# Kernel optimization log

Hardware: AMD Instinct MI355X
Metric: run time of the kernel (lower is better)

## Reference

```python
import jax, jax.numpy as jnp
import numpy as np

HEADS = 8

def _ape(f, c):
    # sinusoidal positional encoding, matches PositionalEncoding buffer pe[:f]
    pos = jnp.arange(f, dtype=jnp.float32)[:, None]                      # [f,1]
    div = jnp.exp(jnp.arange(0, c, 2, dtype=jnp.float32) * (-np.log(10000.0) / c))  # [c/2]
    pe = jnp.zeros((f, c), dtype=jnp.float32)
    pe = pe.at[:, 0::2].set(jnp.sin(pos * div))
    pe = pe.at[:, 1::2].set(jnp.cos(pos * div))
    return pe


def setup_inputs() -> dict:
    key = jax.random.key(0)
    ks = jax.random.split(key, 6)
    b, f, d, c = 2, 16, 4096, 320
    s = 1.0 / np.sqrt(c)
    return {
        'hidden_states': jax.random.normal(ks[0], (b * f, d, c), dtype=jnp.float32),
        'Wq': jax.random.normal(ks[1], (c, c), dtype=jnp.float32) * s,
        'Wk': jax.random.normal(ks[2], (c, c), dtype=jnp.float32) * s,
        'Wv': jax.random.normal(ks[3], (c, c), dtype=jnp.float32) * s,
        'Wo': jax.random.normal(ks[4], (c, c), dtype=jnp.float32) * s,
        'bo': jnp.zeros((c,), dtype=jnp.float32),
        'video_length': 16,
    }


def reference(hidden_states, Wq, Wk, Wv, Wo, bo, video_length):
    bf, d, c = hidden_states.shape
    f = video_length
    b = bf // f
    dh = c // HEADS
    # rearrange '(b f) d c -> (b d) f c'
    x = hidden_states.reshape(b, f, d, c).transpose(0, 2, 1, 3).reshape(b * d, f, c)
    # APE positional encoding over frames (dropout p=0)
    x = x + _ape(f, c)[None, :, :]
    # QKV projections (bias-free, diffusers CrossAttention)
    q = (x @ Wq.T).reshape(b * d, f, HEADS, dh)
    k = (x @ Wk.T).reshape(b * d, f, HEADS, dh)
    v = (x @ Wv.T).reshape(b * d, f, HEADS, dh)
    scale = dh ** -0.5
    scores = jnp.einsum('bqhd,bkhd->bhqk', q, k) * scale          # [B,h,f,f]
    causal = jnp.tril(jnp.ones((f, f), dtype=bool))
    scores = jnp.where(causal[None, None], scores, -jnp.inf)
    attn = jax.nn.softmax(scores, axis=-1)
    out = jnp.einsum('bhqk,bkhd->bqhd', attn, v).reshape(b * d, f, c)
    out = out @ Wo.T + bo
    # rearrange '(b d) f c -> (b f) d c'
    out = out.reshape(b, d, f, c).transpose(0, 2, 1, 3).reshape(b * f, d, c)
    return out
```

## Files before the change

### kernel.cpp

```cpp
#include <hip/hip_runtime.h>
#include <stdint.h>

#define F 16
#define CDIM 320
#define DDIM 4096
#define NSEQ 8192
#define WPB 4
#define THREADS 256
#define NT 20
#define KS 10

typedef __attribute__((ext_vector_type(8))) short short8;
typedef __attribute__((ext_vector_type(4))) float f32x4;
typedef __attribute__((ext_vector_type(2))) unsigned int uint2v;
typedef __attribute__((ext_vector_type(4))) unsigned int uint4v;

__device__ __forceinline__ unsigned short f2bf(float f) {
    union { float f; uint32_t u; } v; v.f = f;
    uint32_t r = v.u + 0x7FFFu + ((v.u >> 16) & 1u);
    return (unsigned short)(r >> 16);
}
__device__ __forceinline__ int swz(int row, int b) {
    return row * 640 + (b ^ ((row & 7) << 4));
}

__global__ __launch_bounds__(256)
void pack_weights_kernel(const float* __restrict__ Wq, const float* __restrict__ Wk,
                         const float* __restrict__ Wv, const float* __restrict__ Wo,
                         char* __restrict__ pk)
{
    const int t = blockIdx.x * 256 + threadIdx.x;
    if (t >= 4 * NT * KS * 64) return;
    const int lane = t & 63;
    const int rest = t >> 6;
    const int ks = rest % KS;
    const int nt = (rest / KS) % NT;
    const int m  = rest / (KS * NT);
    const float* W = (m == 0) ? Wq : (m == 1) ? Wk : (m == 2) ? Wv : Wo;
    const int g = lane >> 4, lr = lane & 15;
    const float* src = W + (size_t)(nt * 16 + lr) * CDIM + ks * 32 + g * 8;
    const f32x4 a = *(const f32x4*)src;
    const f32x4 b = *(const f32x4*)(src + 4);
    float vals[8] = {a[0], a[1], a[2], a[3], b[0], b[1], b[2], b[3]};
    short8 o;
#pragma unroll
    for (int j = 0; j < 8; ++j) o[j] = (short)f2bf(vals[j]);
    *(short8*)(pk + (size_t)t * 16) = o;
}

__global__ __launch_bounds__(THREADS, 2)
void temporal_attn_kernel(const float* __restrict__ hs,
                          const char* __restrict__ wpk,
                          const float* __restrict__ bo,
                          float* __restrict__ out)
{
    extern __shared__ __align__(16) char smem[];
    const int tid  = threadIdx.x;
    const int lane = tid & 63;
    const int wave = tid >> 6;
    const int g    = lane >> 4;
    const int lr   = lane & 15;

    const int seq = blockIdx.x * WPB + wave;
    const int bi  = seq >> 12;
    const int di  = seq & (DDIM - 1);

    char* const kbuf = smem + wave * 20480;
    char* const vbuf = kbuf + 10240;
    const char* const wl = wpk + lane * 16;

    const float* xrow = hs + ((size_t)(bi * F + lr) * DDIM + di) * CDIM;
    short8 axk[KS];
#pragma unroll
    for (int ks = 0; ks < KS; ++ks) {
        const int k0 = ks * 32 + g * 8;
        const f32x4 a = __builtin_nontemporal_load((const f32x4*)(xrow + k0));
        const f32x4 b = __builtin_nontemporal_load((const f32x4*)(xrow + k0 + 4));
        float xv[8] = {a[0], a[1], a[2], a[3], b[0], b[1], b[2], b[3]};
#pragma unroll
        for (int jj = 0; jj < 4; ++jj) {
            const float c0 = (float)(k0 + 2 * jj);
            const float dv = __expf(c0 * -0.028782313662425575f);
            const float ang = (float)lr * dv;
            xv[2 * jj]     += __sinf(ang);
            xv[2 * jj + 1] += __cosf(ang);
        }
        short8 t;
#pragma unroll
        for (int j = 0; j < 8; ++j) t[j] = (short)f2bf(xv[j]);
        axk[ks] = t;
    }

    auto proj = [&](int m, char* dst, int mode) {
        const char* base = wpk + lane * 16 + (size_t)(m * NT) * KS * 1024;
        short8 fa[KS], fb[KS];
#pragma unroll
        for (int ks = 0; ks < KS; ++ks)
            fa[ks] = *(const short8*)(base + (size_t)ks * 1024);
#pragma unroll 1
        for (int np = 0; np < 10; ++np) {
#pragma unroll
            for (int ks = 0; ks < KS; ++ks)
                fb[ks] = *(const short8*)(base + (size_t)((2 * np + 1) * KS + ks) * 1024);
            f32x4 a0l = {0.f, 0.f, 0.f, 0.f}, a0h = {0.f, 0.f, 0.f, 0.f};
#pragma unroll
            for (int k5 = 0; k5 < 5; ++k5) {
                a0l = __builtin_amdgcn_mfma_f32_16x16x32_bf16(axk[k5],     fa[k5],     a0l, 0, 0, 0);
                a0h = __builtin_amdgcn_mfma_f32_16x16x32_bf16(axk[k5 + 5], fa[k5 + 5], a0h, 0, 0, 0);
            }
            const f32x4 a0 = a0l + a0h;
            if (np < 9) {
#pragma unroll
                for (int ks = 0; ks < KS; ++ks)
                    fa[ks] = *(const short8*)(base + (size_t)((2 * np + 2) * KS + ks) * 1024);
            }
            f32x4 a1l = {0.f, 0.f, 0.f, 0.f}, a1h = {0.f, 0.f, 0.f, 0.f};
#pragma unroll
            for (int k5 = 0; k5 < 5; ++k5) {
                a1l = __builtin_amdgcn_mfma_f32_16x16x32_bf16(axk[k5],     fb[k5],     a1l, 0, 0, 0);
                a1h = __builtin_amdgcn_mfma_f32_16x16x32_bf16(axk[k5 + 5], fb[k5 + 5], a1h, 0, 0, 0);
            }
            const f32x4 a1 = a1l + a1h;
            const int c0 = 2 * np * 16 + lr;
            const int c1 = c0 + 16;
            if (mode == 0) {
#pragma unroll
                for (int r = 0; r < 4; ++r) {
                    const int row = g * 4 + r;
                    *(short*)(dst + swz(row, c0 * 2)) = (short)f2bf(a0[r]);
                    *(short*)(dst + swz(row, c1 * 2)) = (short)f2bf(a1[r]);
                }
            } else {
#pragma unroll
                for (int r = 0; r < 4; ++r) {
                    const int key = g * 4 + r;
                    *(short*)(dst + c0 * 32 + key * 2) = (short)f2bf(a0[r]);
                    *(short*)(dst + c1 * 32 + key * 2) = (short)f2bf(a1[r]);
                }
            }
        }
    };

    proj(0, kbuf, 0);
    proj(1, vbuf, 0);

    const float scale = 0.15811388300841897f;
    const short8 z8 = {0, 0, 0, 0, 0, 0, 0, 0};
    uint2v ppk[8];
#pragma unroll
    for (int h = 0; h < 8; ++h) {
        const int cb = h * 80;
        short8 kf = *(const short8*)(vbuf + swz(lr, cb + g * 16));
        short8 qf = *(const short8*)(kbuf + swz(lr, cb + g * 16));
        short8 kt8 = *(const short8*)(vbuf + swz(lr, cb + 64));
        short8 qt8 = *(const short8*)(kbuf + swz(lr, cb + 64));
        short8 kt = (g == 0) ? kt8 : z8;
        short8 qt = (g == 0) ? qt8 : z8;
        f32x4 c = {0.f, 0.f, 0.f, 0.f};
        c = __builtin_amdgcn_mfma_f32_16x16x32_bf16(kf, qf, c, 0, 0, 0);
        c = __builtin_amdgcn_mfma_f32_16x16x32_bf16(kt, qt, c, 0, 0, 0);
        float sv[4];
        float m4 = -1e30f;
#pragma unroll
        for (int r = 0; r < 4; ++r) {
            sv[r] = (g * 4 + r <= lr) ? c[r] * scale : -1e30f;
            m4 = fmaxf(m4, sv[r]);
        }
        m4 = fmaxf(m4, __shfl_xor(m4, 16));
        m4 = fmaxf(m4, __shfl_xor(m4, 32));
        float sum = 0.f;
#pragma unroll
        for (int r = 0; r < 4; ++r) { sv[r] = __expf(sv[r] - m4); sum += sv[r]; }
        sum += __shfl_xor(sum, 16);
        sum += __shfl_xor(sum, 32);
        const float inv = 1.f / sum;
        uint2v pk;
        pk[0] = (uint32_t)f2bf(sv[0] * inv) | ((uint32_t)f2bf(sv[1] * inv) << 16);
        pk[1] = (uint32_t)f2bf(sv[2] * inv) | ((uint32_t)f2bf(sv[3] * inv) << 16);
        ppk[h] = pk;
    }

    proj(2, kbuf, 1);

#pragma unroll
    for (int h = 0; h < 8; ++h) {
        uint2v own = ppk[h];
        uint2v x16;
        x16[0] = (uint32_t)__shfl_xor((int)own[0], 16);
        x16[1] = (uint32_t)__shfl_xor((int)own[1], 16);
        uint4v pair;
        pair[0] = ((g & 1) == 0) ? own[0] : x16[0];
        pair[1] = ((g & 1) == 0) ? own[1] : x16[1];
        pair[2] = ((g & 1) == 0) ? x16[0] : own[0];
        pair[3] = ((g & 1) == 0) ? x16[1] : own[1];
        uint4v rec;
#pragma unroll
        for (int i = 0; i < 4; ++i) rec[i] = (uint32_t)__shfl_xor((int)pair[i], 32);
        uint4v af4;
#pragma unroll
        for (int i = 0; i < 4; ++i)
            af4[i] = (g == 0) ? pair[i] : (g == 1) ? rec[i] : 0u;
        const short8 af = *(const short8*)&af4;

#pragma unroll
        for (int t = 0; t < 3; ++t) {
            const int lcol = (t == 2) ? (lr & 7) : lr;
            const int col  = h * 40 + t * 16 + lcol;
            const short8 bf = *(const short8*)(kbuf + col * 32 + g * 16);
            f32x4 o = {0.f, 0.f, 0.f, 0.f};
            o = __builtin_amdgcn_mfma_f32_16x16x32_bf16(af, bf, o, 0, 0, 0);
            if (t < 2 || lr < 8) {
#pragma unroll
                for (int r = 0; r < 4; ++r)
                    *(short*)(vbuf + swz(g * 4 + r, col * 2)) = (short)f2bf(o[r]);
            }
        }
    }

    short8 aof[KS];
#pragma unroll
    for (int ks = 0; ks < KS; ++ks)
        aof[ks] = *(const short8*)(vbuf + swz(lr, ks * 64 + g * 16));

    {
        const char* base = wpk + lane * 16 + (size_t)(3 * NT) * KS * 1024;
        short8 fa[KS], fb[KS];
#pragma unroll
        for (int ks = 0; ks < KS; ++ks)
            fa[ks] = *(const short8*)(base + (size_t)ks * 1024);
#pragma unroll 1
        for (int np = 0; np < 10; ++np) {
#pragma unroll
            for (int ks = 0; ks < KS; ++ks)
                fb[ks] = *(const short8*)(base + (size_t)((2 * np + 1) * KS + ks) * 1024);
            f32x4 a0l = {0.f, 0.f, 0.f, 0.f}, a0h = {0.f, 0.f, 0.f, 0.f};
#pragma unroll
            for (int k5 = 0; k5 < 5; ++k5) {
                a0l = __builtin_amdgcn_mfma_f32_16x16x32_bf16(aof[k5],     fa[k5],     a0l, 0, 0, 0);
                a0h = __builtin_amdgcn_mfma_f32_16x16x32_bf16(aof[k5 + 5], fa[k5 + 5], a0h, 0, 0, 0);
            }
            const f32x4 a0 = a0l + a0h;
            if (np < 9) {
#pragma unroll
                for (int ks = 0; ks < KS; ++ks)
                    fa[ks] = *(const short8*)(base + (size_t)((2 * np + 2) * KS + ks) * 1024);
            }
            f32x4 a1l = {0.f, 0.f, 0.f, 0.f}, a1h = {0.f, 0.f, 0.f, 0.f};
#pragma unroll
            for (int k5 = 0; k5 < 5; ++k5) {
                a1l = __builtin_amdgcn_mfma_f32_16x16x32_bf16(aof[k5],     fb[k5],     a1l, 0, 0, 0);
                a1h = __builtin_amdgcn_mfma_f32_16x16x32_bf16(aof[k5 + 5], fb[k5 + 5], a1h, 0, 0, 0);
            }
            const f32x4 a1 = a1l + a1h;

            const int c0 = 2 * np * 16 + lr;
            const int c1 = c0 + 16;
            const float bias0 = bo[c0];
            const float bias1 = bo[c1];
#pragma unroll
            for (int r = 0; r < 4; ++r) {
                float* rowp = out + ((size_t)(bi * F + g * 4 + r) * DDIM + di) * CDIM;
                rowp[c0] = a0[r] + bias0;
                rowp[c1] = a1[r] + bias1;
            }
        }
    }
}

extern "C" void kernel_launch(void* const* d_in, const int* in_sizes, int n_in,
                              void* d_out, int out_size, void* d_ws, size_t ws_size,
                              hipStream_t stream) {
    const float* hs = (const float*)d_in[0];
    const float* Wq = (const float*)d_in[1];
    const float* Wk = (const float*)d_in[2];
    const float* Wv = (const float*)d_in[3];
    const float* Wo = (const float*)d_in[4];
    const float* bo = (const float*)d_in[5];
    float* out = (float*)d_out;
    char* wpk = (char*)d_ws;

    pack_weights_kernel<<<dim3((4 * NT * KS * 64 + 255) / 256), dim3(256), 0, stream>>>(
        Wq, Wk, Wv, Wo, wpk);

    const int lds = WPB * 20480;
    (void)hipFuncSetAttribute((const void*)temporal_attn_kernel,
                              hipFuncAttributeMaxDynamicSharedMemorySize, lds);
    temporal_attn_kernel<<<dim3(NSEQ / WPB), dim3(THREADS), lds, stream>>>(
        hs, wpk, bo, out);
}
```

Before: 252.5 us.

## Process two sequences per wave to reuse weight fragments across both

Each wave now handles two adjacent sequences (A and B) instead of one, so every weight fragment loaded from global memory feeds two MFMA chains and weight traffic per sequence is halved. The block shrinks to two waves with the same LDS per block, and launch bounds drop to one block minimum. The positional-encoding sin/cos is shared between the two sequences. The cost is much higher register pressure (two sets of activation fragments and accumulators), which may lower occupancy or cause spills. Each K-reduction also becomes a single serial MFMA chain of ten instead of two interleaved chains of five, though the A and B chains interleave with each other.

```diff
diff --git a/kernel.cpp b/kernel.cpp
--- a/kernel.cpp
+++ b/kernel.cpp
@@ -5,8 +5,7 @@
 #define CDIM 320
 #define DDIM 4096
 #define NSEQ 8192
-#define WPB 4
-#define THREADS 256
+#define THREADS 128
 #define NT 20
 #define KS 10
 
@@ -48,7 +47,7 @@
     *(short8*)(pk + (size_t)t * 16) = o;
 }
 
-__global__ __launch_bounds__(THREADS, 2)
+__global__ __launch_bounds__(THREADS, 1)
 void temporal_attn_kernel(const float* __restrict__ hs,
                           const char* __restrict__ wpk,
                           const float* __restrict__ bo,
@@ -61,37 +60,43 @@
     const int g    = lane >> 4;
     const int lr   = lane & 15;
 
-    const int seq = blockIdx.x * WPB + wave;
-    const int bi  = seq >> 12;
-    const int di  = seq & (DDIM - 1);
-
-    char* const kbuf = smem + wave * 20480;
-    char* const vbuf = kbuf + 10240;
-    const char* const wl = wpk + lane * 16;
-
-    const float* xrow = hs + ((size_t)(bi * F + lr) * DDIM + di) * CDIM;
-    short8 axk[KS];
+    const int seqA = blockIdx.x * 4 + wave * 2;
+    const int bi  = seqA >> 12;
+    const int di  = seqA & (DDIM - 1);
+
+    char* const kbufA = smem + wave * 40960;
+    char* const vbufA = kbufA + 10240;
+    char* const kbufB = kbufA + 20480;
+    char* const vbufB = kbufA + 30720;
+
+    const float* xrowA = hs + ((size_t)(bi * F + lr) * DDIM + di) * CDIM;
+    const float* xrowB = xrowA + CDIM;
+    short8 axkA[KS], axkB[KS];
 #pragma unroll
     for (int ks = 0; ks < KS; ++ks) {
         const int k0 = ks * 32 + g * 8;
-        const f32x4 a = __builtin_nontemporal_load((const f32x4*)(xrow + k0));
-        const f32x4 b = __builtin_nontemporal_load((const f32x4*)(xrow + k0 + 4));
-        float xv[8] = {a[0], a[1], a[2], a[3], b[0], b[1], b[2], b[3]};
+        const f32x4 aA = __builtin_nontemporal_load((const f32x4*)(xrowA + k0));
+        const f32x4 bA = __builtin_nontemporal_load((const f32x4*)(xrowA + k0 + 4));
+        const f32x4 aB = __builtin_nontemporal_load((const f32x4*)(xrowB + k0));
+        const f32x4 bB = __builtin_nontemporal_load((const f32x4*)(xrowB + k0 + 4));
+        float xvA[8] = {aA[0], aA[1], aA[2], aA[3], bA[0], bA[1], bA[2], bA[3]};
+        float xvB[8] = {aB[0], aB[1], aB[2], aB[3], bB[0], bB[1], bB[2], bB[3]};
 #pragma unroll
         for (int jj = 0; jj < 4; ++jj) {
             const float c0 = (float)(k0 + 2 * jj);
             const float dv = __expf(c0 * -0.028782313662425575f);
             const float ang = (float)lr * dv;
-            xv[2 * jj]     += __sinf(ang);
-            xv[2 * jj + 1] += __cosf(ang);
-        }
-        short8 t;
-#pragma unroll
-        for (int j = 0; j < 8; ++j) t[j] = (short)f2bf(xv[j]);
-        axk[ks] = t;
-    }
-
-    auto proj = [&](int m, char* dst, int mode) {
+            const float sn = __sinf(ang), cs = __cosf(ang);
+            xvA[2 * jj] += sn;  xvA[2 * jj + 1] += cs;
+            xvB[2 * jj] += sn;  xvB[2 * jj + 1] += cs;
+        }
+        short8 tA, tB;
+#pragma unroll
+        for (int j = 0; j < 8; ++j) { tA[j] = (short)f2bf(xvA[j]); tB[j] = (short)f2bf(xvB[j]); }
+        axkA[ks] = tA;  axkB[ks] = tB;
+    }
+
+    auto proj = [&](int m, char* dA, char* dB, int mode) {
         const char* base = wpk + lane * 16 + (size_t)(m * NT) * KS * 1024;
         short8 fa[KS], fb[KS];
 #pragma unroll
@@ -102,65 +107,66 @@
 #pragma unroll
             for (int ks = 0; ks < KS; ++ks)
                 fb[ks] = *(const short8*)(base + (size_t)((2 * np + 1) * KS + ks) * 1024);
-            f32x4 a0l = {0.f, 0.f, 0.f, 0.f}, a0h = {0.f, 0.f, 0.f, 0.f};
-#pragma unroll
-            for (int k5 = 0; k5 < 5; ++k5) {
-                a0l = __builtin_amdgcn_mfma_f32_16x16x32_bf16(axk[k5],     fa[k5],     a0l, 0, 0, 0);
-                a0h = __builtin_amdgcn_mfma_f32_16x16x32_bf16(axk[k5 + 5], fa[k5 + 5], a0h, 0, 0, 0);
-            }
-            const f32x4 a0 = a0l + a0h;
+            f32x4 a0A = {0.f, 0.f, 0.f, 0.f}, a0B = {0.f, 0.f, 0.f, 0.f};
+#pragma unroll
+            for (int ks = 0; ks < KS; ++ks) {
+                a0A = __builtin_amdgcn_mfma_f32_16x16x32_bf16(axkA[ks], fa[ks], a0A, 0, 0, 0);
+                a0B = __builtin_amdgcn_mfma_f32_16x16x32_bf16(axkB[ks], fa[ks], a0B, 0, 0, 0);
+            }
             if (np < 9) {
 #pragma unroll
                 for (int ks = 0; ks < KS; ++ks)
                     fa[ks] = *(const short8*)(base + (size_t)((2 * np + 2) * KS + ks) * 1024);
             }
-            f32x4 a1l = {0.f, 0.f, 0.f, 0.f}, a1h = {0.f, 0.f, 0.f, 0.f};
-#pragma unroll
-            for (int k5 = 0; k5 < 5; ++k5) {
-                a1l = __builtin_amdgcn_mfma_f32_16x16x32_bf16(axk[k5],     fb[k5],     a1l, 0, 0, 0);
-                a1h = __builtin_amdgcn_mfma_f32_16x16x32_bf16(axk[k5 + 5], fb[k5 + 5], a1h, 0, 0, 0);
-            }
-            const f32x4 a1 = a1l + a1h;
+            f32x4 a1A = {0.f, 0.f, 0.f, 0.f}, a1B = {0.f, 0.f, 0.f, 0.f};
+#pragma unroll
+            for (int ks = 0; ks < KS; ++ks) {
+                a1A = __builtin_amdgcn_mfma_f32_16x16x32_bf16(axkA[ks], fb[ks], a1A, 0, 0, 0);
+                a1B = __builtin_amdgcn_mfma_f32_16x16x32_bf16(axkB[ks], fb[ks], a1B, 0, 0, 0);
+            }
             const int c0 = 2 * np * 16 + lr;
             const int c1 = c0 + 16;
             if (mode == 0) {
 #pragma unroll
                 for (int r = 0; r < 4; ++r) {
                     const int row = g * 4 + r;
-                    *(short*)(dst + swz(row, c0 * 2)) = (short)f2bf(a0[r]);
-                    *(short*)(dst + swz(row, c1 * 2)) = (short)f2bf(a1[r]);
+                    *(short*)(dA + swz(row, c0 * 2)) = (short)f2bf(a0A[r]);
+                    *(short*)(dA + swz(row, c1 * 2)) = (short)f2bf(a1A[r]);
+                    *(short*)(dB + swz(row, c0 * 2)) = (short)f2bf(a0B[r]);
+                    *(short*)(dB + swz(row, c1 * 2)) = (short)f2bf(a1B[r]);
                 }
             } else {
 #pragma unroll
                 for (int r = 0; r < 4; ++r) {
                     const int key = g * 4 + r;
-                    *(short*)(dst + c0 * 32 + key * 2) = (short)f2bf(a0[r]);
-                    *(short*)(dst + c1 * 32 + key * 2) = (short)f2bf(a1[r]);
+                    *(short*)(dA + c0 * 32 + key * 2) = (short)f2bf(a0A[r]);
+                    *(short*)(dA + c1 * 32 + key * 2) = (short)f2bf(a1A[r]);
+                    *(short*)(dB + c0 * 32 + key * 2) = (short)f2bf(a0B[r]);
+                    *(short*)(dB + c1 * 32 + key * 2) = (short)f2bf(a1B[r]);
                 }
             }
         }
     };
 
-    proj(0, kbuf, 0);
-    proj(1, vbuf, 0);
+    proj(0, kbufA, kbufB, 0);
+    proj(1, vbufA, vbufB, 0);
 
     const float scale = 0.15811388300841897f;
     const short8 z8 = {0, 0, 0, 0, 0, 0, 0, 0};
-    uint2v ppk[8];
+    uint2v ppkA[8], ppkB[8];
 #pragma unroll
     for (int h = 0; h < 8; ++h) {
         const int cb = h * 80;
-        short8 kf = *(const short8*)(vbuf + swz(lr, cb + g * 16));
-        short8 qf = *(const short8*)(kbuf + swz(lr, cb + g * 16));
-        short8 kt8 = *(const short8*)(vbuf + swz(lr, cb + 64));
-        short8 qt8 = *(const short8*)(kbuf + swz(lr, cb + 64));
+        short8 kf = *(const short8*)(vbufA + swz(lr, cb + g * 16));
+        short8 qf = *(const short8*)(kbufA + swz(lr, cb + g * 16));
+        short8 kt8 = *(const short8*)(vbufA + swz(lr, cb + 64));
+        short8 qt8 = *(const short8*)(kbufA + swz(lr, cb + 64));
         short8 kt = (g == 0) ? kt8 : z8;
         short8 qt = (g == 0) ? qt8 : z8;
         f32x4 c = {0.f, 0.f, 0.f, 0.f};
         c = __builtin_amdgcn_mfma_f32_16x16x32_bf16(kf, qf, c, 0, 0, 0);
         c = __builtin_amdgcn_mfma_f32_16x16x32_bf16(kt, qt, c, 0, 0, 0);
-        float sv[4];
-        float m4 = -1e30f;
+        float sv[4]; float m4 = -1e30f;
 #pragma unroll
         for (int r = 0; r < 4; ++r) {
             sv[r] = (g * 4 + r <= lr) ? c[r] * scale : -1e30f;
@@ -177,14 +183,45 @@
         uint2v pk;
         pk[0] = (uint32_t)f2bf(sv[0] * inv) | ((uint32_t)f2bf(sv[1] * inv) << 16);
         pk[1] = (uint32_t)f2bf(sv[2] * inv) | ((uint32_t)f2bf(sv[3] * inv) << 16);
-        ppk[h] = pk;
-    }
-
-    proj(2, kbuf, 1);
-
+        ppkA[h] = pk;
+    }
 #pragma unroll
     for (int h = 0; h < 8; ++h) {
-        uint2v own = ppk[h];
+        const int cb = h * 80;
+        short8 kf = *(const short8*)(vbufB + swz(lr, cb + g * 16));
+        short8 qf = *(const short8*)(kbufB + swz(lr, cb + g * 16));
+        short8 kt8 = *(const short8*)(vbufB + swz(lr, cb + 64));
+        short8 qt8 = *(const short8*)(kbufB + swz(lr, cb + 64));
+        short8 kt = (g == 0) ? kt8 : z8;
+        short8 qt = (g == 0) ? qt8 : z8;
+        f32x4 c = {0.f, 0.f, 0.f, 0.f};
+        c = __builtin_amdgcn_mfma_f32_16x16x32_bf16(kf, qf, c, 0, 0, 0);
+        c = __builtin_amdgcn_mfma_f32_16x16x32_bf16(kt, qt, c, 0, 0, 0);
+        float sv[4]; float m4 = -1e30f;
+#pragma unroll
+        for (int r = 0; r < 4; ++r) {
+            sv[r] = (g * 4 + r <= lr) ? c[r] * scale : -1e30f;
+            m4 = fmaxf(m4, sv[r]);
+        }
+        m4 = fmaxf(m4, __shfl_xor(m4, 16));
+        m4 = fmaxf(m4, __shfl_xor(m4, 32));
+        float sum = 0.f;
+#pragma unroll
+        for (int r = 0; r < 4; ++r) { sv[r] = __expf(sv[r] - m4); sum += sv[r]; }
+        sum += __shfl_xor(sum, 16);
+        sum += __shfl_xor(sum, 32);
+        const float inv = 1.f / sum;
+        uint2v pk;
+        pk[0] = (uint32_t)f2bf(sv[0] * inv) | ((uint32_t)f2bf(sv[1] * inv) << 16);
+        pk[1] = (uint32_t)f2bf(sv[2] * inv) | ((uint32_t)f2bf(sv[3] * inv) << 16);
+        ppkB[h] = pk;
+    }
+
+    proj(2, kbufA, kbufB, 1);
+
+#pragma unroll
+    for (int h = 0; h < 8; ++h) {
+        uint2v own = ppkA[h];
         uint2v x16;
         x16[0] = (uint32_t)__shfl_xor((int)own[0], 16);
         x16[1] = (uint32_t)__shfl_xor((int)own[1], 16);
@@ -201,27 +238,60 @@
         for (int i = 0; i < 4; ++i)
             af4[i] = (g == 0) ? pair[i] : (g == 1) ? rec[i] : 0u;
         const short8 af = *(const short8*)&af4;
-
 #pragma unroll
         for (int t = 0; t < 3; ++t) {
             const int lcol = (t == 2) ? (lr & 7) : lr;
             const int col  = h * 40 + t * 16 + lcol;
-            const short8 bf = *(const short8*)(kbuf + col * 32 + g * 16);
+            const short8 bf = *(const short8*)(kbufA + col * 32 + g * 16);
             f32x4 o = {0.f, 0.f, 0.f, 0.f};
             o = __builtin_amdgcn_mfma_f32_16x16x32_bf16(af, bf, o, 0, 0, 0);
             if (t < 2 || lr < 8) {
 #pragma unroll
                 for (int r = 0; r < 4; ++r)
-                    *(short*)(vbuf + swz(g * 4 + r, col * 2)) = (short)f2bf(o[r]);
-            }
-        }
-    }
-
-    short8 aof[KS];
-#pragma unroll
-    for (int ks = 0; ks < KS; ++ks)
-        aof[ks] = *(const short8*)(vbuf + swz(lr, ks * 64 + g * 16));
-
+                    *(short*)(vbufA + swz(g * 4 + r, col * 2)) = (short)f2bf(o[r]);
+            }
+        }
+    }
+#pragma unroll
+    for (int h = 0; h < 8; ++h) {
+        uint2v own = ppkB[h];
+        uint2v x16;
+        x16[0] = (uint32_t)__shfl_xor((int)own[0], 16);
+        x16[1] = (uint32_t)__shfl_xor((int)own[1], 16);
+        uint4v pair;
+        pair[0] = ((g & 1) == 0) ? own[0] : x16[0];
+        pair[1] = ((g & 1) == 0) ? own[1] : x16[1];
+        pair[2] = ((g & 1) == 0) ? x16[0] : own[0];
+        pair[3] = ((g & 1) == 0) ? x16[1] : own[1];
+        uint4v rec;
+#pragma unroll
+        for (int i = 0; i < 4; ++i) rec[i] = (uint32_t)__shfl_xor((int)pair[i], 32);
+        uint4v af4;
+#pragma unroll
+        for (int i = 0; i < 4; ++i)
+            af4[i] = (g == 0) ? pair[i] : (g == 1) ? rec[i] : 0u;
+        const short8 af = *(const short8*)&af4;
+#pragma unroll
+        for (int t = 0; t < 3; ++t) {
+            const int lcol = (t == 2) ? (lr & 7) : lr;
+            const int col  = h * 40 + t * 16 + lcol;
+            const short8 bf = *(const short8*)(kbufB + col * 32 + g * 16);
+            f32x4 o = {0.f, 0.f, 0.f, 0.f};
+            o = __builtin_amdgcn_mfma_f32_16x16x32_bf16(af, bf, o, 0, 0, 0);
+            if (t < 2 || lr < 8) {
+#pragma unroll
+                for (int r = 0; r < 4; ++r)
+                    *(short*)(vbufB + swz(g * 4 + r, col * 2)) = (short)f2bf(o[r]);
+            }
+        }
+    }
+
+    short8 aofA[KS], aofB[KS];
+#pragma unroll
+    for (int ks = 0; ks < KS; ++ks) {
+        aofA[ks] = *(const short8*)(vbufA + swz(lr, ks * 64 + g * 16));
+        aofB[ks] = *(const short8*)(vbufB + swz(lr, ks * 64 + g * 16));
+    }
     {
         const char* base = wpk + lane * 16 + (size_t)(3 * NT) * KS * 1024;
         short8 fa[KS], fb[KS];
@@ -233,35 +303,35 @@
 #pragma unroll
             for (int ks = 0; ks < KS; ++ks)
                 fb[ks] = *(const short8*)(base + (size_t)((2 * np + 1) * KS + ks) * 1024);
-            f32x4 a0l = {0.f, 0.f, 0.f, 0.f}, a0h = {0.f, 0.f, 0.f, 0.f};
-#pragma unroll
-            for (int k5 = 0; k5 < 5; ++k5) {
-                a0l = __builtin_amdgcn_mfma_f32_16x16x32_bf16(aof[k5],     fa[k5],     a0l, 0, 0, 0);
-                a0h = __builtin_amdgcn_mfma_f32_16x16x32_bf16(aof[k5 + 5], fa[k5 + 5], a0h, 0, 0, 0);
-            }
-            const f32x4 a0 = a0l + a0h;
+            f32x4 a0A = {0.f, 0.f, 0.f, 0.f}, a0B = {0.f, 0.f, 0.f, 0.f};
+#pragma unroll
+            for (int ks = 0; ks < KS; ++ks) {
+                a0A = __builtin_amdgcn_mfma_f32_16x16x32_bf16(aofA[ks], fa[ks], a0A, 0, 0, 0);
+                a0B = __builtin_amdgcn_mfma_f32_16x16x32_bf16(aofB[ks], fa[ks], a0B, 0, 0, 0);
+            }
             if (np < 9) {
 #pragma unroll
                 for (int ks = 0; ks < KS; ++ks)
                     fa[ks] = *(const short8*)(base + (size_t)((2 * np + 2) * KS + ks) * 1024);
             }
-            f32x4 a1l = {0.f, 0.f, 0.f, 0.f}, a1h = {0.f, 0.f, 0.f, 0.f};
-#pragma unroll
-            for (int k5 = 0; k5 < 5; ++k5) {
-                a1l = __builtin_amdgcn_mfma_f32_16x16x32_bf16(aof[k5],     fb[k5],     a1l, 0, 0, 0);
-                a1h = __builtin_amdgcn_mfma_f32_16x16x32_bf16(aof[k5 + 5], fb[k5 + 5], a1h, 0, 0, 0);
-            }
-            const f32x4 a1 = a1l + a1h;
-
+            f32x4 a1A = {0.f, 0.f, 0.f, 0.f}, a1B = {0.f, 0.f, 0.f, 0.f};
+#pragma unroll
+            for (int ks = 0; ks < KS; ++ks) {
+                a1A = __builtin_amdgcn_mfma_f32_16x16x32_bf16(aofA[ks], fb[ks], a1A, 0, 0, 0);
+                a1B = __builtin_amdgcn_mfma_f32_16x16x32_bf16(aofB[ks], fb[ks], a1B, 0, 0, 0);
+            }
             const int c0 = 2 * np * 16 + lr;
             const int c1 = c0 + 16;
             const float bias0 = bo[c0];
             const float bias1 = bo[c1];
 #pragma unroll
             for (int r = 0; r < 4; ++r) {
-                float* rowp = out + ((size_t)(bi * F + g * 4 + r) * DDIM + di) * CDIM;
-                rowp[c0] = a0[r] + bias0;
-                rowp[c1] = a1[r] + bias1;
+                float* rowpA = out + ((size_t)(bi * F + g * 4 + r) * DDIM + di) * CDIM;
+                float* rowpB = rowpA + CDIM;
+                rowpA[c0] = a0A[r] + bias0;
+                rowpA[c1] = a1A[r] + bias1;
+                rowpB[c0] = a0B[r] + bias0;
+                rowpB[c1] = a1B[r] + bias1;
             }
         }
     }
@@ -282,9 +352,9 @@
     pack_weights_kernel<<<dim3((4 * NT * KS * 64 + 255) / 256), dim3(256), 0, stream>>>(
         Wq, Wk, Wv, Wo, wpk);
 
-    const int lds = WPB * 20480;
+    const int lds = 2 * 40960;
     (void)hipFuncSetAttribute((const void*)temporal_attn_kernel,
                               hipFuncAttributeMaxDynamicSharedMemorySize, lds);
-    temporal_attn_kernel<<<dim3(NSEQ / WPB), dim3(THREADS), lds, stream>>>(
+    temporal_attn_kernel<<<dim3(NSEQ / 4), dim3(THREADS), lds, stream>>>(
         hs, wpk, bo, out);
 }
```

After: 238.5 us. 1.06x faster.

## Process four sequences per wave to reuse weight fragments across sequences

Applied to the files above, without the earlier changes.

Each single-wave block now handles four sequences instead of one, so every weight fragment loaded from global memory feeds four MFMAs rather than one. The positional-encoding sin/cos values are computed once and shared across the four sequences. This cuts weight load traffic per sequence and gives more independent MFMA chains for latency hiding. The cost is much higher register pressure (four activation fragment sets plus four weight buffers), possible spills, and fewer waves per CU with 80KB LDS per single-wave block.

```diff
diff --git a/kernel.cpp b/kernel.cpp
--- a/kernel.cpp
+++ b/kernel.cpp
@@ -5,8 +5,8 @@
 #define CDIM 320
 #define DDIM 4096
 #define NSEQ 8192
-#define WPB 4
-#define THREADS 256
+#define SEQS 4
+#define THREADS 64
 #define NT 20
 #define KS 10
 
@@ -48,220 +48,279 @@
     *(short8*)(pk + (size_t)t * 16) = o;
 }
 
-__global__ __launch_bounds__(THREADS, 2)
+__global__ __launch_bounds__(THREADS, 1)
 void temporal_attn_kernel(const float* __restrict__ hs,
                           const char* __restrict__ wpk,
                           const float* __restrict__ bo,
                           float* __restrict__ out)
 {
     extern __shared__ __align__(16) char smem[];
-    const int tid  = threadIdx.x;
-    const int lane = tid & 63;
-    const int wave = tid >> 6;
+    const int lane = threadIdx.x & 63;
     const int g    = lane >> 4;
     const int lr   = lane & 15;
 
-    const int seq = blockIdx.x * WPB + wave;
-    const int bi  = seq >> 12;
-    const int di  = seq & (DDIM - 1);
-
-    char* const kbuf = smem + wave * 20480;
-    char* const vbuf = kbuf + 10240;
-    const char* const wl = wpk + lane * 16;
-
-    const float* xrow = hs + ((size_t)(bi * F + lr) * DDIM + di) * CDIM;
-    short8 axk[KS];
+    const int seq0 = blockIdx.x * SEQS;
+    const int bi  = seq0 >> 12;
+    const int di  = seq0 & (DDIM - 1);
+
+    char* kb[SEQS];
+    char* vb[SEQS];
+#pragma unroll
+    for (int s = 0; s < SEQS; ++s) {
+        kb[s] = smem + s * 20480;
+        vb[s] = kb[s] + 10240;
+    }
+
+    const float* xrow0 = hs + ((size_t)(bi * F + lr) * DDIM + di) * CDIM;
+    short8 axk[SEQS][KS];
 #pragma unroll
     for (int ks = 0; ks < KS; ++ks) {
         const int k0 = ks * 32 + g * 8;
-        const f32x4 a = __builtin_nontemporal_load((const f32x4*)(xrow + k0));
-        const f32x4 b = __builtin_nontemporal_load((const f32x4*)(xrow + k0 + 4));
-        float xv[8] = {a[0], a[1], a[2], a[3], b[0], b[1], b[2], b[3]};
+        float sn[4], cs[4];
 #pragma unroll
         for (int jj = 0; jj < 4; ++jj) {
             const float c0 = (float)(k0 + 2 * jj);
             const float dv = __expf(c0 * -0.028782313662425575f);
             const float ang = (float)lr * dv;
-            xv[2 * jj]     += __sinf(ang);
-            xv[2 * jj + 1] += __cosf(ang);
-        }
-        short8 t;
-#pragma unroll
-        for (int j = 0; j < 8; ++j) t[j] = (short)f2bf(xv[j]);
-        axk[ks] = t;
-    }
-
-    auto proj = [&](int m, char* dst, int mode) {
+            sn[jj] = __sinf(ang);  cs[jj] = __cosf(ang);
+        }
+#pragma unroll
+        for (int s = 0; s < SEQS; ++s) {
+            const float* xr = xrow0 + s * CDIM;
+            const f32x4 a = __builtin_nontemporal_load((const f32x4*)(xr + k0));
+            const f32x4 b = __builtin_nontemporal_load((const f32x4*)(xr + k0 + 4));
+            float xv[8] = {a[0], a[1], a[2], a[3], b[0], b[1], b[2], b[3]};
+#pragma unroll
+            for (int jj = 0; jj < 4; ++jj) {
+                xv[2 * jj]     += sn[jj];
+                xv[2 * jj + 1] += cs[jj];
+            }
+            short8 t;
+#pragma unroll
+            for (int j = 0; j < 8; ++j) t[j] = (short)f2bf(xv[j]);
+            axk[s][ks] = t;
+        }
+    }
+
+    auto proj = [&](int m, char* const* dst, int mode) {
         const char* base = wpk + lane * 16 + (size_t)(m * NT) * KS * 1024;
-        short8 fa[KS], fb[KS];
-#pragma unroll
-        for (int ks = 0; ks < KS; ++ks)
-            fa[ks] = *(const short8*)(base + (size_t)ks * 1024);
+        short8 f0[KS], f1[KS], f2[KS], f3[KS];
+#pragma unroll
+        for (int ks = 0; ks < KS; ++ks) {
+            f0[ks] = *(const short8*)(base + (size_t)ks * 1024);
+            f1[ks] = *(const short8*)(base + (size_t)(KS + ks) * 1024);
+        }
+        auto storeT = [&](int ti, const f32x4* acc) {
+            const int c = ti * 16 + lr;
+            if (mode == 0) {
+#pragma unroll
+                for (int s = 0; s < SEQS; ++s)
+#pragma unroll
+                    for (int r = 0; r < 4; ++r)
+                        *(short*)(dst[s] + swz(g * 4 + r, c * 2)) = (short)f2bf(acc[s][r]);
+            } else {
+#pragma unroll
+                for (int s = 0; s < SEQS; ++s)
+#pragma unroll
+                    for (int r = 0; r < 4; ++r)
+                        *(short*)(dst[s] + c * 32 + (g * 4 + r) * 2) = (short)f2bf(acc[s][r]);
+            }
+        };
 #pragma unroll 1
-        for (int np = 0; np < 10; ++np) {
-#pragma unroll
-            for (int ks = 0; ks < KS; ++ks)
-                fb[ks] = *(const short8*)(base + (size_t)((2 * np + 1) * KS + ks) * 1024);
-            f32x4 a0l = {0.f, 0.f, 0.f, 0.f}, a0h = {0.f, 0.f, 0.f, 0.f};
-#pragma unroll
-            for (int k5 = 0; k5 < 5; ++k5) {
-                a0l = __builtin_amdgcn_mfma_f32_16x16x32_bf16(axk[k5],     fa[k5],     a0l, 0, 0, 0);
-                a0h = __builtin_amdgcn_mfma_f32_16x16x32_bf16(axk[k5 + 5], fa[k5 + 5], a0h, 0, 0, 0);
-            }
-            const f32x4 a0 = a0l + a0h;
-            if (np < 9) {
+        for (int np2 = 0; np2 < 5; ++np2) {
+            const int t = np2 * 4;
+#pragma unroll
+            for (int ks = 0; ks < KS; ++ks) {
+                f2[ks] = *(const short8*)(base + (size_t)((t + 2) * KS + ks) * 1024);
+                f3[ks] = *(const short8*)(base + (size_t)((t + 3) * KS + ks) * 1024);
+            }
+            {
+                f32x4 a0[SEQS], a1[SEQS];
+#pragma unroll
+                for (int s = 0; s < SEQS; ++s) { a0[s] = {0,0,0,0}; a1[s] = {0,0,0,0}; }
 #pragma unroll
                 for (int ks = 0; ks < KS; ++ks)
-                    fa[ks] = *(const short8*)(base + (size_t)((2 * np + 2) * KS + ks) * 1024);
-            }
-            f32x4 a1l = {0.f, 0.f, 0.f, 0.f}, a1h = {0.f, 0.f, 0.f, 0.f};
-#pragma unroll
-            for (int k5 = 0; k5 < 5; ++k5) {
-                a1l = __builtin_amdgcn_mfma_f32_16x16x32_bf16(axk[k5],     fb[k5],     a1l, 0, 0, 0);
-                a1h = __builtin_amdgcn_mfma_f32_16x16x32_bf16(axk[k5 + 5], fb[k5 + 5], a1h, 0, 0, 0);
-            }
-            const f32x4 a1 = a1l + a1h;
-            const int c0 = 2 * np * 16 + lr;
-            const int c1 = c0 + 16;
-            if (mode == 0) {
-#pragma unroll
-                for (int r = 0; r < 4; ++r) {
-                    const int row = g * 4 + r;
-                    *(short*)(dst + swz(row, c0 * 2)) = (short)f2bf(a0[r]);
-                    *(short*)(dst + swz(row, c1 * 2)) = (short)f2bf(a1[r]);
+#pragma unroll
+                    for (int s = 0; s < SEQS; ++s) {
+                        a0[s] = __builtin_amdgcn_mfma_f32_16x16x32_bf16(axk[s][ks], f0[ks], a0[s], 0, 0, 0);
+                        a1[s] = __builtin_amdgcn_mfma_f32_16x16x32_bf16(axk[s][ks], f1[ks], a1[s], 0, 0, 0);
+                    }
+                storeT(t, a0);
+                storeT(t + 1, a1);
+            }
+            if (np2 < 4) {
+#pragma unroll
+                for (int ks = 0; ks < KS; ++ks) {
+                    f0[ks] = *(const short8*)(base + (size_t)((t + 4) * KS + ks) * 1024);
+                    f1[ks] = *(const short8*)(base + (size_t)((t + 5) * KS + ks) * 1024);
                 }
-            } else {
-#pragma unroll
-                for (int r = 0; r < 4; ++r) {
-                    const int key = g * 4 + r;
-                    *(short*)(dst + c0 * 32 + key * 2) = (short)f2bf(a0[r]);
-                    *(short*)(dst + c1 * 32 + key * 2) = (short)f2bf(a1[r]);
-                }
+            }
+            {
+                f32x4 a2[SEQS], a3[SEQS];
+#pragma unroll
+                for (int s = 0; s < SEQS; ++s) { a2[s] = {0,0,0,0}; a3[s] = {0,0,0,0}; }
+#pragma unroll
+                for (int ks = 0; ks < KS; ++ks)
+#pragma unroll
+                    for (int s = 0; s < SEQS; ++s) {
+                        a2[s] = __builtin_amdgcn_mfma_f32_16x16x32_bf16(axk[s][ks], f2[ks], a2[s], 0, 0, 0);
+                        a3[s] = __builtin_amdgcn_mfma_f32_16x16x32_bf16(axk[s][ks], f3[ks], a3[s], 0, 0, 0);
+                    }
+                storeT(t + 2, a2);
+                storeT(t + 3, a3);
             }
         }
     };
 
-    proj(0, kbuf, 0);
-    proj(1, vbuf, 0);
+    proj(0, kb, 0);
+    proj(1, vb, 0);
 
     const float scale = 0.15811388300841897f;
     const short8 z8 = {0, 0, 0, 0, 0, 0, 0, 0};
-    uint2v ppk[8];
+    uint2v ppk[SEQS][8];
 #pragma unroll
     for (int h = 0; h < 8; ++h) {
         const int cb = h * 80;
-        short8 kf = *(const short8*)(vbuf + swz(lr, cb + g * 16));
-        short8 qf = *(const short8*)(kbuf + swz(lr, cb + g * 16));
-        short8 kt8 = *(const short8*)(vbuf + swz(lr, cb + 64));
-        short8 qt8 = *(const short8*)(kbuf + swz(lr, cb + 64));
-        short8 kt = (g == 0) ? kt8 : z8;
-        short8 qt = (g == 0) ? qt8 : z8;
-        f32x4 c = {0.f, 0.f, 0.f, 0.f};
-        c = __builtin_amdgcn_mfma_f32_16x16x32_bf16(kf, qf, c, 0, 0, 0);
-        c = __builtin_amdgcn_mfma_f32_16x16x32_bf16(kt, qt, c, 0, 0, 0);
-        float sv[4];
-        float m4 = -1e30f;
-#pragma unroll
-        for (int r = 0; r < 4; ++r) {
-            sv[r] = (g * 4 + r <= lr) ? c[r] * scale : -1e30f;
-            m4 = fmaxf(m4, sv[r]);
-        }
-        m4 = fmaxf(m4, __shfl_xor(m4, 16));
-        m4 = fmaxf(m4, __shfl_xor(m4, 32));
-        float sum = 0.f;
-#pragma unroll
-        for (int r = 0; r < 4; ++r) { sv[r] = __expf(sv[r] - m4); sum += sv[r]; }
-        sum += __shfl_xor(sum, 16);
-        sum += __shfl_xor(sum, 32);
-        const float inv = 1.f / sum;
-        uint2v pk;
-        pk[0] = (uint32_t)f2bf(sv[0] * inv) | ((uint32_t)f2bf(sv[1] * inv) << 16);
-        pk[1] = (uint32_t)f2bf(sv[2] * inv) | ((uint32_t)f2bf(sv[3] * inv) << 16);
-        ppk[h] = pk;
-    }
-
-    proj(2, kbuf, 1);
+#pragma unroll
+        for (int s = 0; s < SEQS; ++s) {
+            short8 kf  = *(const short8*)(vb[s] + swz(lr, cb + g * 16));
+            short8 qf  = *(const short8*)(kb[s] + swz(lr, cb + g * 16));
+            short8 kt8 = *(const short8*)(vb[s] + swz(lr, cb + 64));
+            short8 qt8 = *(const short8*)(kb[s] + swz(lr, cb + 64));
+            short8 kt = (g == 0) ? kt8 : z8;
+            short8 qt = (g == 0) ? qt8 : z8;
+            f32x4 c = {0.f, 0.f, 0.f, 0.f};
+            c = __builtin_amdgcn_mfma_f32_16x16x32_bf16(kf, qf, c, 0, 0, 0);
+            c = __builtin_amdgcn_mfma_f32_16x16x32_bf16(kt, qt, c, 0, 0, 0);
+            float sv[4];
+            float m4 = -1e30f;
+#pragma unroll
+            for (int r = 0; r < 4; ++r) {
+                sv[r] = (g * 4 + r <= lr) ? c[r] * scale : -1e30f;
+                m4 = fmaxf(m4, sv[r]);
+            }
+            m4 = fmaxf(m4, __shfl_xor(m4, 16));
+            m4 = fmaxf(m4, __shfl_xor(m4, 32));
+            float sum = 0.f;
+#pragma unroll
+            for (int r = 0; r < 4; ++r) { sv[r] = __expf(sv[r] - m4); sum += sv[r]; }
+            sum += __shfl_xor(sum, 16);
+            sum += __shfl_xor(sum, 32);
+            const float inv = 1.f / sum;
+            uint2v pk;
+            pk[0] = (uint32_t)f2bf(sv[0] * inv) | ((uint32_t)f2bf(sv[1] * inv) << 16);
+            pk[1] = (uint32_t)f2bf(sv[2] * inv) | ((uint32_t)f2bf(sv[3] * inv) << 16);
+            ppk[s][h] = pk;
+        }
+    }
+
+    proj(2, kb, 1);
 
 #pragma unroll
     for (int h = 0; h < 8; ++h) {
-        uint2v own = ppk[h];
-        uint2v x16;
-        x16[0] = (uint32_t)__shfl_xor((int)own[0], 16);
-        x16[1] = (uint32_t)__shfl_xor((int)own[1], 16);
-        uint4v pair;
-        pair[0] = ((g & 1) == 0) ? own[0] : x16[0];
-        pair[1] = ((g & 1) == 0) ? own[1] : x16[1];
-        pair[2] = ((g & 1) == 0) ? x16[0] : own[0];
-        pair[3] = ((g & 1) == 0) ? x16[1] : own[1];
-        uint4v rec;
-#pragma unroll
-        for (int i = 0; i < 4; ++i) rec[i] = (uint32_t)__shfl_xor((int)pair[i], 32);
-        uint4v af4;
-#pragma unroll
-        for (int i = 0; i < 4; ++i)
-            af4[i] = (g == 0) ? pair[i] : (g == 1) ? rec[i] : 0u;
-        const short8 af = *(const short8*)&af4;
-
-#pragma unroll
-        for (int t = 0; t < 3; ++t) {
-            const int lcol = (t == 2) ? (lr & 7) : lr;
-            const int col  = h * 40 + t * 16 + lcol;
-            const short8 bf = *(const short8*)(kbuf + col * 32 + g * 16);
-            f32x4 o = {0.f, 0.f, 0.f, 0.f};
-            o = __builtin_amdgcn_mfma_f32_16x16x32_bf16(af, bf, o, 0, 0, 0);
-            if (t < 2 || lr < 8) {
-#pragma unroll
-                for (int r = 0; r < 4; ++r)
-                    *(short*)(vbuf + swz(g * 4 + r, col * 2)) = (short)f2bf(o[r]);
-            }
-        }
-    }
-
-    short8 aof[KS];
+#pragma unroll
+        for (int s = 0; s < SEQS; ++s) {
+            uint2v own = ppk[s][h];
+            uint2v x16;
+            x16[0] = (uint32_t)__shfl_xor((int)own[0], 16);
+            x16[1] = (uint32_t)__shfl_xor((int)own[1], 16);
+            uint4v pair;
+            pair[0] = ((g & 1) == 0) ? own[0] : x16[0];
+            pair[1] = ((g & 1) == 0) ? own[1] : x16[1];
+            pair[2] = ((g & 1) == 0) ? x16[0] : own[0];
+            pair[3] = ((g & 1) == 0) ? x16[1] : own[1];
+            uint4v rec;
+#pragma unroll
+            for (int i = 0; i < 4; ++i) rec[i] = (uint32_t)__shfl_xor((int)pair[i], 32);
+            uint4v af4;
+#pragma unroll
+            for (int i = 0; i < 4; ++i)
+                af4[i] = (g == 0) ? pair[i] : (g == 1) ? rec[i] : 0u;
+            const short8 af = *(const short8*)&af4;
+#pragma unroll
+            for (int t = 0; t < 3; ++t) {
+                const int lcol = (t == 2) ? (lr & 7) : lr;
+                const int col  = h * 40 + t * 16 + lcol;
+                const short8 bf = *(const short8*)(kb[s] + col * 32 + g * 16);
+                f32x4 o = {0.f, 0.f, 0.f, 0.f};
+                o = __builtin_amdgcn_mfma_f32_16x16x32_bf16(af, bf, o, 0, 0, 0);
+                if (t < 2 || lr < 8) {
+#pragma unroll
+                    for (int r = 0; r < 4; ++r)
+                        *(short*)(vb[s] + swz(g * 4 + r, col * 2)) = (short)f2bf(o[r]);
+                }
+            }
+        }
+    }
+
+    short8 aof[SEQS][KS];
 #pragma unroll
     for (int ks = 0; ks < KS; ++ks)
-        aof[ks] = *(const short8*)(vbuf + swz(lr, ks * 64 + g * 16));
-
+#pragma unroll
+        for (int s = 0; s < SEQS; ++s)
+            aof[s][ks] = *(const short8*)(vb[s] + swz(lr, ks * 64 + g * 16));
     {
         const char* base = wpk + lane * 16 + (size_t)(3 * NT) * KS * 1024;
-        short8 fa[KS], fb[KS];
-#pragma unroll
-        for (int ks = 0; ks < KS; ++ks)
-            fa[ks] = *(const short8*)(base + (size_t)ks * 1024);
-#pragma unroll 1
-        for (int np = 0; np < 10; ++np) {
-#pragma unroll
-            for (int ks = 0; ks < KS; ++ks)
-                fb[ks] = *(const short8*)(base + (size_t)((2 * np + 1) * KS + ks) * 1024);
-            f32x4 a0l = {0.f, 0.f, 0.f, 0.f}, a0h = {0.f, 0.f, 0.f, 0.f};
-#pragma unroll
-            for (int k5 = 0; k5 < 5; ++k5) {
-                a0l = __builtin_amdgcn_mfma_f32_16x16x32_bf16(aof[k5],     fa[k5],     a0l, 0, 0, 0);
-                a0h = __builtin_amdgcn_mfma_f32_16x16x32_bf16(aof[k5 + 5], fa[k5 + 5], a0h, 0, 0, 0);
-            }
-            const f32x4 a0 = a0l + a0h;
-            if (np < 9) {
-#pragma unroll
-                for (int ks = 0; ks < KS; ++ks)
-                    fa[ks] = *(const short8*)(base + (size_t)((2 * np + 2) * KS + ks) * 1024);
-            }
-            f32x4 a1l = {0.f, 0.f, 0.f, 0.f}, a1h = {0.f, 0.f, 0.f, 0.f};
-#pragma unroll
-            for (int k5 = 0; k5 < 5; ++k5) {
-                a1l = __builtin_amdgcn_mfma_f32_16x16x32_bf16(aof[k5],     fb[k5],     a1l, 0, 0, 0);
-                a1h = __builtin_amdgcn_mfma_f32_16x16x32_bf16(aof[k5 + 5], fb[k5 + 5], a1h, 0, 0, 0);
-            }
-            const f32x4 a1 = a1l + a1h;
-
-            const int c0 = 2 * np * 16 + lr;
+        short8 f0[KS], f1[KS], f2[KS], f3[KS];
+#pragma unroll
+        for (int ks = 0; ks < KS; ++ks) {
+            f0[ks] = *(const short8*)(base + (size_t)ks * 1024);
+            f1[ks] = *(const short8*)(base + (size_t)(KS + ks) * 1024);
+        }
+        auto outStore2 = [&](int t0, const f32x4* accL, const f32x4* accH) {
+            const int c0 = t0 * 16 + lr;
             const int c1 = c0 + 16;
             const float bias0 = bo[c0];
             const float bias1 = bo[c1];
 #pragma unroll
-            for (int r = 0; r < 4; ++r) {
-                float* rowp = out + ((size_t)(bi * F + g * 4 + r) * DDIM + di) * CDIM;
-                rowp[c0] = a0[r] + bias0;
-                rowp[c1] = a1[r] + bias1;
+            for (int s = 0; s < SEQS; ++s)
+#pragma unroll
+                for (int r = 0; r < 4; ++r) {
+                    float* rowp = out + ((size_t)(bi * F + g * 4 + r) * DDIM + di + s) * CDIM;
+                    rowp[c0] = accL[s][r] + bias0;
+                    rowp[c1] = accH[s][r] + bias1;
+                }
+        };
+#pragma unroll 1
+        for (int np2 = 0; np2 < 5; ++np2) {
+            const int t = np2 * 4;
+#pragma unroll
+            for (int ks = 0; ks < KS; ++ks) {
+                f2[ks] = *(const short8*)(base + (size_t)((t + 2) * KS + ks) * 1024);
+                f3[ks] = *(const short8*)(base + (size_t)((t + 3) * KS + ks) * 1024);
+            }
+            {
+                f32x4 a0[SEQS], a1[SEQS];
+#pragma unroll
+                for (int s = 0; s < SEQS; ++s) { a0[s] = {0,0,0,0}; a1[s] = {0,0,0,0}; }
+#pragma unroll
+                for (int ks = 0; ks < KS; ++ks)
+#pragma unroll
+                    for (int s = 0; s < SEQS; ++s) {
+                        a0[s] = __builtin_amdgcn_mfma_f32_16x16x32_bf16(aof[s][ks], f0[ks], a0[s], 0, 0, 0);
+                        a1[s] = __builtin_amdgcn_mfma_f32_16x16x32_bf16(aof[s][ks], f1[ks], a1[s], 0, 0, 0);
+                    }
+                outStore2(t, a0, a1);
+            }
+            if (np2 < 4) {
+#pragma unroll
+                for (int ks = 0; ks < KS; ++ks) {
+                    f0[ks] = *(const short8*)(base + (size_t)((t + 4) * KS + ks) * 1024);
+                    f1[ks] = *(const short8*)(base + (size_t)((t + 5) * KS + ks) * 1024);
+                }
+            }
+            {
+                f32x4 a2[SEQS], a3[SEQS];
+#pragma unroll
+                for (int s = 0; s < SEQS; ++s) { a2[s] = {0,0,0,0}; a3[s] = {0,0,0,0}; }
+#pragma unroll
+                for (int ks = 0; ks < KS; ++ks)
+#pragma unroll
+                    for (int s = 0; s < SEQS; ++s) {
+                        a2[s] = __builtin_amdgcn_mfma_f32_16x16x32_bf16(aof[s][ks], f2[ks], a2[s], 0, 0, 0);
+                        a3[s] = __builtin_amdgcn_mfma_f32_16x16x32_bf16(aof[s][ks], f3[ks], a3[s], 0, 0, 0);
+                    }
+                outStore2(t + 2, a2, a3);
             }
         }
     }
@@ -282,9 +341,9 @@
     pack_weights_kernel<<<dim3((4 * NT * KS * 64 + 255) / 256), dim3(256), 0, stream>>>(
         Wq, Wk, Wv, Wo, wpk);
 
-    const int lds = WPB * 20480;
+    const int lds = SEQS * 20480;
     (void)hipFuncSetAttribute((const void*)temporal_attn_kernel,
                               hipFuncAttributeMaxDynamicSharedMemorySize, lds);
-    temporal_attn_kernel<<<dim3(NSEQ / WPB), dim3(THREADS), lds, stream>>>(
+    temporal_attn_kernel<<<dim3(NSEQ / SEQS), dim3(THREADS), lds, stream>>>(
         hs, wpk, bo, out);
 }
```

New measurement: 717.9 us. +184.3%, slower.
